# Optimization experiments

Measured on AMD Instinct MI355X. Metric: run time of the kernel, lower is better.

Reference implementation:

```python
import jax, jax.numpy as jnp
import numpy as np

B, N = 32, 4096
SA1 = (512, 0.2, 32)   # npoint, radius, nsample
SA2 = (128, 0.4, 64)
MLP1 = [3, 64, 64, 128]
MLP2 = [131, 128, 128, 256]   # 128 feats + 3 relative xyz
MLP3 = [259, 256, 512, 1024]  # 256 feats + 3 xyz (group_all)


def _mk_mlp(key, dims, prefix, d):
    for i in range(len(dims) - 1):
        key, k1 = jax.random.split(key)
        d[f"{prefix}_w{i}"] = jax.random.normal(k1, (dims[i], dims[i + 1]), jnp.float32) * (1.0 / np.sqrt(dims[i]))
        d[f"{prefix}_b{i}"] = jnp.zeros((dims[i + 1],), jnp.float32)
    return key


def setup_inputs() -> dict:
    key = jax.random.key(0)
    d = {}
    key, kx = jax.random.split(key)
    d["xyz"] = jax.random.uniform(kx, (B, N, 3), jnp.float32)  # normalized coords in [0,1)
    key = _mk_mlp(key, MLP1, "sa1", d)
    key = _mk_mlp(key, MLP2, "sa2", d)
    key = _mk_mlp(key, MLP3, "sa3", d)
    key, k1, k2 = jax.random.split(key, 3)
    d["cls_w"] = jax.random.normal(k1, (1024, 1), jnp.float32) * 0.03
    d["cls_b"] = jnp.zeros((1,), jnp.float32)
    d["reg_w"] = jax.random.normal(k2, (1024, 4), jnp.float32) * 0.03
    d["reg_b"] = jnp.zeros((4,), jnp.float32)
    return d


def fps(xyz, npoint):
    """Farthest point sampling. xyz: (B,N,3) -> idx (B,npoint) int32."""
    Bb, Nn, _ = xyz.shape

    def step(carry, _):
        dist, farthest = carry  # (B,N), (B,)
        centroid = jnp.take_along_axis(xyz, farthest[:, None, None], axis=1)  # (B,1,3)
        d = jnp.sum((xyz - centroid) ** 2, axis=-1)  # (B,N)
        dist = jnp.minimum(dist, d)
        nxt = jnp.argmax(dist, axis=-1).astype(jnp.int32)
        return (dist, nxt), farthest

    init = (jnp.full((Bb, Nn), 1e10, xyz.dtype), jnp.zeros((Bb,), jnp.int32))
    _, idx = jax.lax.scan(step, init, None, length=npoint)
    return idx.T  # (B,npoint)


def ball_query(radius, nsample, xyz, new_xyz):
    """xyz: (B,N,3), new_xyz: (B,S,3) -> idx (B,S,nsample) int32."""
    Bb, S, _ = new_xyz.shape
    Nn = xyz.shape[1]
    sqr = jnp.sum((new_xyz[:, :, None, :] - xyz[:, None, :, :]) ** 2, axis=-1)  # (B,S,N)
    idx = jnp.broadcast_to(jnp.arange(Nn, dtype=jnp.int32), (Bb, S, Nn))
    idx = jnp.where(sqr > radius * radius, Nn, idx)
    idx = jnp.sort(idx, axis=-1)[:, :, :nsample]
    first = idx[:, :, :1]
    return jnp.where(idx == Nn, first, idx)  # pad out-of-ball slots with first neighbor


def _sa(xyz, feats, npoint, radius, nsample, ws, bs):
    Bb = xyz.shape[0]
    cidx = fps(xyz, npoint)
    new_xyz = xyz[jnp.arange(Bb)[:, None], cidx]  # (B,S,3)
    gidx = ball_query(radius, nsample, xyz, new_xyz)  # (B,S,K)
    b3 = jnp.arange(Bb)[:, None, None]
    g = xyz[b3, gidx] - new_xyz[:, :, None, :]  # (B,S,K,3) relative coords
    if feats is not None:
        g = jnp.concatenate([g, feats[b3, gidx]], axis=-1)
    for w, b in zip(ws, bs):
        g = jax.nn.relu(g @ w + b)
    return new_xyz, jnp.max(g, axis=2)  # (B,S,C_out)


def _sa_all(xyz, feats, ws, bs):
    g = jnp.concatenate([xyz, feats], axis=-1)[:, None]  # (B,1,S,3+C)
    for w, b in zip(ws, bs):
        g = jax.nn.relu(g @ w + b)
    return jnp.max(g, axis=2)[:, 0]  # (B,C_out)


def reference(xyz, sa1_w0, sa1_b0, sa1_w1, sa1_b1, sa1_w2, sa1_b2,
              sa2_w0, sa2_b0, sa2_w1, sa2_b1, sa2_w2, sa2_b2,
              sa3_w0, sa3_b0, sa3_w1, sa3_b1, sa3_w2, sa3_b2,
              cls_w, cls_b, reg_w, reg_b):
    xyz1, f1 = _sa(xyz, None, SA1[0], SA1[1], SA1[2],
                   [sa1_w0, sa1_w1, sa1_w2], [sa1_b0, sa1_b1, sa1_b2])
    xyz2, f2 = _sa(xyz1, f1, SA2[0], SA2[1], SA2[2],
                   [sa2_w0, sa2_w1, sa2_w2], [sa2_b0, sa2_b1, sa2_b2])
    feat = _sa_all(xyz2, f2, [sa3_w0, sa3_w1, sa3_w2], [sa3_b0, sa3_b1, sa3_b2])  # (B,1024)
    return feat @ cls_w + cls_b, feat @ reg_w + reg_b
```

## Files before the change

kernel.cpp:

```cpp
#include <hip/hip_runtime.h>

#define DEVINL __device__ __forceinline__

typedef __attribute__((ext_vector_type(8))) short bf16x8;
typedef __attribute__((ext_vector_type(8))) unsigned short u16x8;
typedef __attribute__((ext_vector_type(4))) float f32x4;

DEVINL unsigned short f2bh(float f){
  unsigned u = __float_as_uint(f);
  return (unsigned short)((u + 0x7FFFu + ((u >> 16) & 1u)) >> 16);
}
DEVINL float bh2f(unsigned short h){ return __uint_as_float(((unsigned)h) << 16); }

DEVINL unsigned long long dpp_max_u64(unsigned long long k) {
#define DPP_STEP(ctrl)                                                        \
  {                                                                           \
    int hi = (int)(k >> 32), lo = (int)(unsigned)k;                           \
    int oh = __builtin_amdgcn_update_dpp(0, hi, ctrl, 0xF, 0xF, 1);           \
    int ol = __builtin_amdgcn_update_dpp(0, lo, ctrl, 0xF, 0xF, 1);           \
    unsigned long long ok =                                                   \
        ((unsigned long long)(unsigned)oh << 32) | (unsigned)ol;              \
    if (ok > k) k = ok;                                                       \
  }
  DPP_STEP(0x111)
  DPP_STEP(0x112)
  DPP_STEP(0x114)
  DPP_STEP(0x118)
  DPP_STEP(0x142)
  DPP_STEP(0x143)
#undef DPP_STEP
  return k;
}

template<int N, int NP, int NT>
DEVINL void fps_body(const float* __restrict__ xyz, float* __restrict__ nxyz,
                     int b, int t) {
  constexpr int PTS = N / NT;
  constexpr int NW = NT / 64;
  __shared__ float xs[N], ys[N], zs[N];
  __shared__ int farr[NP];
  __shared__ unsigned long long sk[2][(NW > 1 ? NW : 1)];
  float px[PTS], py[PTS], pz[PTS], dst[PTS];
  const float* base = xyz + (size_t)b * N * 3;
#pragma unroll
  for (int j = 0; j < PTS; ++j) {
    int i = t + j * NT;
    float x = base[i * 3 + 0], y = base[i * 3 + 1], z = base[i * 3 + 2];
    px[j] = x; py[j] = y; pz[j] = z;
    xs[i] = x; ys[i] = y; zs[i] = z;
    dst[j] = 1e10f;
  }
  if constexpr (NW > 1) __syncthreads();
  int far = 0;
  const int wv = t >> 6, ln = t & 63;
  for (int s = 0; s < NP; ++s) {
    float cx = xs[far], cy = ys[far], cz = zs[far];
    if (t == 0) farr[s] = far;
    float bv = -1.f; int bi = 0;
#pragma unroll
    for (int j = 0; j < PTS; ++j) {
      float dx = __fsub_rn(px[j], cx), dy = __fsub_rn(py[j], cy), dz = __fsub_rn(pz[j], cz);
      float d = __fadd_rn(__fadd_rn(__fmul_rn(dx, dx), __fmul_rn(dy, dy)), __fmul_rn(dz, dz));
      float nd = fminf(dst[j], d);
      dst[j] = nd;
      int i = t + j * NT;
      if (nd > bv) { bv = nd; bi = i; }
    }
    unsigned long long key =
        ((unsigned long long)__float_as_uint(bv) << 32) | (unsigned)(~bi);
    key = dpp_max_u64(key);
    if constexpr (NW == 1) {
      int rl = __builtin_amdgcn_readlane((int)(unsigned)key, 63);
      far = (int)(~(unsigned)rl);
    } else {
      const int p = s & 1;
      if (ln == 63) sk[p][wv] = key;
      __syncthreads();
      unsigned long long m = sk[p][0];
#pragma unroll
      for (int q = 1; q < NW; ++q) {
        unsigned long long qk = sk[p][q];
        if (qk > m) m = qk;
      }
      far = (int)(~(unsigned)m);
    }
  }
  if constexpr (NW > 1) __syncthreads();
  for (int s2 = t; s2 < NP; s2 += NT) {
    int fi = farr[s2];
    float* o = nxyz + ((size_t)b * NP + s2) * 3;
    o[0] = xs[fi]; o[1] = ys[fi]; o[2] = zs[fi];
  }
}

template<int N, int NS>
DEVINL void bq_body(const float* __restrict__ pts, const float* __restrict__ centers,
                    int* __restrict__ gidx, int Q, float r2, int blk, int t) {
  const int wv = t >> 6, ln = t & 63;
  const int g = blk * 4 + wv;
  const int b = g / Q, q = g % Q;
  const float* pb = pts + (size_t)b * N * 3;
  const float* c = centers + ((size_t)b * Q + q) * 3;
  const float cx = c[0], cy = c[1], cz = c[2];
  __shared__ int gbuf[4][NS];
  int taken = 0;
  for (int base = 0; base < N; base += 64) {
    if (taken >= NS) break;
    int i = base + ln;
    float dx = __fsub_rn(pb[i * 3 + 0], cx), dy = __fsub_rn(pb[i * 3 + 1], cy),
          dz = __fsub_rn(pb[i * 3 + 2], cz);
    float d = __fadd_rn(__fadd_rn(__fmul_rn(dx, dx), __fmul_rn(dy, dy)), __fmul_rn(dz, dz));
    bool in = (d <= r2);
    unsigned long long mk = __ballot(in);
    int rank = __popcll(mk & ((1ull << ln) - 1ull));
    int pos = taken + rank;
    if (in && pos < NS) gbuf[wv][pos] = i;
    taken += (int)__popcll(mk);
  }
  int total = taken < NS ? taken : NS;
  int first = gbuf[wv][0];
  int* out = gidx + ((size_t)b * Q + q) * NS;
  for (int j = ln; j < NS; j += 64) out[j] = (j < total) ? gbuf[wv][j] : first;
}

struct WPEnt { const float* W; unsigned short* hi; unsigned short* lo; int K, N, row0, beg, end; };
struct WPTab { WPEnt e[8]; };
DEVINL void wprep_body(const WPTab& tab, int idx) {
#pragma unroll
  for (int i = 0; i < 8; ++i) {
    const WPEnt& E = tab.e[i];
    if (idx >= E.beg && idx < E.end) {
      int local = idx - E.beg;
      int k = local / E.N, n = local - k * E.N;
      float v = E.W[(size_t)(E.row0 + k) * E.N + n];
      unsigned short h = f2bh(v);
      E.hi[(size_t)n * E.K + k] = h;
      E.lo[(size_t)n * E.K + k] = f2bh(v - bh2f(h));
    }
  }
}

__global__ __launch_bounds__(256) void fps1_wprep_kernel(const float* __restrict__ xyz,
                                                         float* __restrict__ nx1, WPTab tab) {
  if (blockIdx.x < 32) { fps_body<4096, 512, 256>(xyz, nx1, blockIdx.x, threadIdx.x); return; }
  wprep_body(tab, (blockIdx.x - 32) * 256 + threadIdx.x);
}

__global__ __launch_bounds__(256) void fps2_bq1_kernel(const float* __restrict__ xyz,
                                                       const float* __restrict__ nx1,
                                                       int* __restrict__ gidx1,
                                                       float* __restrict__ nx2, float r21) {
  if (blockIdx.x < 32) {
    if (threadIdx.x < 64) fps_body<512, 128, 64>(nx1, nx2, blockIdx.x, threadIdx.x);
    return;
  }
  bq_body<4096, 32>(xyz, nx1, gidx1, 512, r21, blockIdx.x - 32, threadIdx.x);
}

template<int K, int N, int AS, int WS, bool XYZC, int NTH>
DEVINL void do_layer(const unsigned short* __restrict__ Ghi, const unsigned short* __restrict__ Glo,
                     const float* __restrict__ Wxyz,
                     const float* __restrict__ A, unsigned short* __restrict__ Whi,
                     unsigned short* __restrict__ Wlo, const float* __restrict__ sxyz,
                     f32x4* acc, int t) {
  constexpr int KT = K / 32;
  constexpr int NCH = N / 64;
  constexpr int K8 = K / 8;
  constexpr int SI = (64 * K8) / NTH;
  const int l = t & 63, wv = t >> 6;

  u16x8 rh[SI], rl[SI];
#pragma unroll
  for (int s = 0; s < SI; ++s) {
    int u = t + s * NTH;
    int nn = u / K8, k8 = (u - nn * K8) * 8;
    rh[s] = *reinterpret_cast<const u16x8*>(Ghi + (size_t)nn * K + k8);
    rl[s] = *reinterpret_cast<const u16x8*>(Glo + (size_t)nn * K + k8);
  }

  bf16x8 ahi[KT], alo[KT];
  {
    const int row = wv * 16 + (l & 15);
    const float* ap = A + row * AS + (l >> 4) * 8;
#pragma unroll
    for (int kt = 0; kt < KT; ++kt) {
      float4 v0 = *reinterpret_cast<const float4*>(ap + kt * 32);
      float4 v1 = *reinterpret_cast<const float4*>(ap + kt * 32 + 4);
      float f[8] = {v0.x, v0.y, v0.z, v0.w, v1.x, v1.y, v1.z, v1.w};
      bf16x8 h, lo2;
#pragma unroll
      for (int j = 0; j < 8; ++j) {
        unsigned short hb = f2bh(f[j]);
        h[j] = (short)hb;
        lo2[j] = (short)f2bh(f[j] - bh2f(hb));
      }
      ahi[kt] = h; alo[kt] = lo2;
    }
  }
#pragma unroll
  for (int i = 0; i < N / 16; ++i) acc[i] = f32x4{0.f, 0.f, 0.f, 0.f};

#pragma unroll
  for (int c = 0; c < NCH; ++c) {
    __syncthreads();
#pragma unroll
    for (int s = 0; s < SI; ++s) {
      int u = t + s * NTH;
      int nn = u / K8, k8 = (u - nn * K8) * 8;
      *reinterpret_cast<u16x8*>(Whi + nn * WS + k8) = rh[s];
      *reinterpret_cast<u16x8*>(Wlo + nn * WS + k8) = rl[s];
    }
    if (c + 1 < NCH) {
#pragma unroll
      for (int s = 0; s < SI; ++s) {
        int u = t + s * NTH;
        int nn = u / K8, k8 = (u - nn * K8) * 8;
        rh[s] = *reinterpret_cast<const u16x8*>(Ghi + (size_t)((c + 1) * 64 + nn) * K + k8);
        rl[s] = *reinterpret_cast<const u16x8*>(Glo + (size_t)((c + 1) * 64 + nn) * K + k8);
      }
    }
    __syncthreads();
#pragma unroll
    for (int ct = 0; ct < 4; ++ct) {
      const unsigned short* wp = Whi + (ct * 16 + (l & 15)) * WS + (l >> 4) * 8;
      const unsigned short* wq = Wlo + (ct * 16 + (l & 15)) * WS + (l >> 4) * 8;
      f32x4 a = acc[c * 4 + ct];
#pragma unroll
      for (int kt = 0; kt < KT; ++kt) {
        bf16x8 wh = *reinterpret_cast<const bf16x8*>(wp + kt * 32);
        bf16x8 wl = *reinterpret_cast<const bf16x8*>(wq + kt * 32);
        a = __builtin_amdgcn_mfma_f32_16x16x32_bf16(ahi[kt], wh, a, 0, 0, 0);
        a = __builtin_amdgcn_mfma_f32_16x16x32_bf16(alo[kt], wh, a, 0, 0, 0);
        a = __builtin_amdgcn_mfma_f32_16x16x32_bf16(ahi[kt], wl, a, 0, 0, 0);
      }
      acc[c * 4 + ct] = a;
    }
  }
  if constexpr (XYZC) {
    float xr[4][3];
#pragma unroll
    for (int r = 0; r < 4; ++r) {
      int row = wv * 16 + (l >> 4) * 4 + r;
      xr[r][0] = sxyz[row * 4 + 0];
      xr[r][1] = sxyz[row * 4 + 1];
      xr[r][2] = sxyz[row * 4 + 2];
    }
#pragma unroll
    for (int gt = 0; gt < N / 16; ++gt) {
      int col = gt * 16 + (l & 15);
      float w0 = Wxyz[col], w1 = Wxyz[N + col], w2 = Wxyz[2 * N + col];
#pragma unroll
      for (int r = 0; r < 4; ++r)
        acc[gt][r] += xr[r][0] * w0 + xr[r][1] * w1 + xr[r][2] * w2;
    }
  }
}

template<int NPTS, int Q, int M, int GPB, int FD, int C1, int C2, int C3>
__global__ __launch_bounds__(512) void sa2_kernel(
    const float* __restrict__ pts, const float* __restrict__ centers,
    const int* __restrict__ gidx, const float* __restrict__ feats,
    const float* __restrict__ W0, const float* __restrict__ B0,
    const unsigned short* __restrict__ G0h, const unsigned short* __restrict__ G0l,
    const unsigned short* __restrict__ G1h, const unsigned short* __restrict__ G1l,
    const float* __restrict__ B1,
    const unsigned short* __restrict__ G2h, const unsigned short* __restrict__ G2l,
    const float* __restrict__ B2,
    float* __restrict__ fout) {
  constexpr int NTH = 512;
  constexpr int ROWS = M * GPB;
  constexpr int NWV = NTH / 64;
  static_assert(ROWS == 16 * NWV, "wave owns 16 rows");
  constexpr int MK1 = (FD > C1 ? FD : C1);
  constexpr int MAXK = (MK1 > C2 ? MK1 : C2);
  constexpr int AS = MAXK + 12;
  constexpr int WS = MAXK + 8;
  __shared__ __align__(16) float A[ROWS * AS];
  __shared__ __align__(16) unsigned short Whi[64 * WS];
  __shared__ __align__(16) unsigned short Wlo[64 * WS];
  __shared__ float sxyz[ROWS * 4];
  __shared__ int idxs[ROWS];
  __shared__ float ctr[GPB][4];
  __shared__ float red[NWV][C3];

  const int t = threadIdx.x;
  const int blk = blockIdx.x;
  const int b = blk / (Q / GPB);
  const int q0 = (blk % (Q / GPB)) * GPB;
  const int l = t & 63, wv = t >> 6;

  if (t < GPB * 3) {
    int g = t / 3, c2 = t % 3;
    ctr[g][c2] = centers[((size_t)b * Q + q0 + g) * 3 + c2];
  }
  for (int m = t; m < ROWS; m += NTH)
    idxs[m] = gidx[((size_t)b * Q + q0 + (m / M)) * M + (m % M)];
  __syncthreads();
  const float* pb = pts + (size_t)b * NPTS * 3;
  for (int m = t; m < ROWS; m += NTH) {
    int g = m / M, i = idxs[m];
    sxyz[m * 4 + 0] = pb[i * 3 + 0] - ctr[g][0];
    sxyz[m * 4 + 1] = pb[i * 3 + 1] - ctr[g][1];
    sxyz[m * 4 + 2] = pb[i * 3 + 2] - ctr[g][2];
  }
  {
    const int m = t >> 2, co = (t & 3) * (FD / 4);
    const float* src = feats + ((size_t)b * NPTS + idxs[m]) * FD + co;
    float* dst = A + m * AS + co;
#pragma unroll
    for (int j = 0; j < FD / 4; j += 4)
      *reinterpret_cast<float4*>(dst + j) = *reinterpret_cast<const float4*>(src + j);
  }
  __syncthreads();

  f32x4 acc[C3 / 16];

  do_layer<FD, C1, AS, WS, true, NTH>(G0h, G0l, W0, A, Whi, Wlo, sxyz, acc, t);
#pragma unroll
  for (int gt = 0; gt < C1 / 16; ++gt) {
    int col = gt * 16 + (l & 15);
    float bia = B0[col];
#pragma unroll
    for (int r = 0; r < 4; ++r)
      A[(wv * 16 + (l >> 4) * 4 + r) * AS + col] = fmaxf(acc[gt][r] + bia, 0.f);
  }

  do_layer<C1, C2, AS, WS, false, NTH>(G1h, G1l, nullptr, A, Whi, Wlo, sxyz, acc, t);
#pragma unroll
  for (int gt = 0; gt < C2 / 16; ++gt) {
    int col = gt * 16 + (l & 15);
    float bia = B1[col];
#pragma unroll
    for (int r = 0; r < 4; ++r)
      A[(wv * 16 + (l >> 4) * 4 + r) * AS + col] = fmaxf(acc[gt][r] + bia, 0.f);
  }

  do_layer<C2, C3, AS, WS, false, NTH>(G2h, G2l, nullptr, A, Whi, Wlo, sxyz, acc, t);
#pragma unroll
  for (int gt = 0; gt < C3 / 16; ++gt) {
    int col = gt * 16 + (l & 15);
    float v = fmaxf(fmaxf(acc[gt][0], acc[gt][1]), fmaxf(acc[gt][2], acc[gt][3]));
    v = fmaxf(v, __shfl_xor(v, 16, 64));
    v = fmaxf(v, __shfl_xor(v, 32, 64));
    if (l < 16) red[wv][col] = v + B2[col];
  }
  __syncthreads();
  constexpr int WPG = NWV / GPB;
  for (int u = t; u < GPB * C3; u += NTH) {
    int g = u / C3, c2 = u - g * C3;
    float v = red[g * WPG][c2];
#pragma unroll
    for (int w = 1; w < WPG; ++w) v = fmaxf(v, red[g * WPG + w][c2]);
    fout[((size_t)b * Q + q0 + g) * C3 + c2] = fmaxf(v, 0.f);
  }
}

template<int NPTS, int Q, int M, int GPB, int TPB>
DEVINL void sa1_body(const float* __restrict__ pts, const float* __restrict__ centers,
                     const int* __restrict__ gidx,
                     const float* __restrict__ W0, const float* __restrict__ B0,
                     const unsigned short* __restrict__ G1h, const unsigned short* __restrict__ G1l,
                     const float* __restrict__ B1,
                     const unsigned short* __restrict__ G2h, const unsigned short* __restrict__ G2l,
                     const float* __restrict__ B2,
                     float* __restrict__ fout, int sblk, int t) {
  static_assert(M * GPB == 64, "");
  constexpr int C1 = 64, C2 = 64, C3 = 128;
  constexpr int AS = 76;
  constexpr int WS = 72;
  constexpr int NC = C2 + C3;
  __shared__ __align__(16) float A[64 * AS];
  __shared__ __align__(16) unsigned short Wh[NC * WS];
  __shared__ __align__(16) unsigned short Wl[NC * WS];
  __shared__ float sxyz[64 * 4];
  __shared__ int idxs[64];
  __shared__ float ctr[GPB][4];
  __shared__ float red[4][C3];

  const int l = t & 63, wv = t >> 6;

  for (int u = t; u < NC * 8; u += 256) {
    int col = u >> 3, k8 = (u & 7) * 8;
    const unsigned short* sh = (col < C2) ? G1h + (size_t)col * 64 + k8
                                          : G2h + (size_t)(col - C2) * 64 + k8;
    const unsigned short* sl = (col < C2) ? G1l + (size_t)col * 64 + k8
                                          : G2l + (size_t)(col - C2) * 64 + k8;
    *reinterpret_cast<u16x8*>(Wh + col * WS + k8) = *reinterpret_cast<const u16x8*>(sh);
    *reinterpret_cast<u16x8*>(Wl + col * WS + k8) = *reinterpret_cast<const u16x8*>(sl);
  }

  for (int it = 0; it < TPB; ++it) {
    const int blk = sblk * TPB + it;
    const int b = blk / (Q / GPB);
    const int q0 = (blk % (Q / GPB)) * GPB;

    if (t < GPB * 3) {
      int g = t / 3, c2 = t % 3;
      ctr[g][c2] = centers[((size_t)b * Q + q0 + g) * 3 + c2];
    }
    for (int m = t; m < 64; m += 256)
      idxs[m] = gidx[((size_t)b * Q + q0 + (m / M)) * M + (m % M)];
    __syncthreads();
    const float* pb = pts + (size_t)b * NPTS * 3;
    for (int m = t; m < 64; m += 256) {
      int g = m / M, i = idxs[m];
      sxyz[m * 4 + 0] = pb[i * 3 + 0] - ctr[g][0];
      sxyz[m * 4 + 1] = pb[i * 3 + 1] - ctr[g][1];
      sxyz[m * 4 + 2] = pb[i * 3 + 2] - ctr[g][2];
    }
    __syncthreads();

    for (int u = t; u < 64 * C1; u += 256) {
      int m = u / C1, c2 = u - m * C1;
      float v = B0[c2] + sxyz[m * 4 + 0] * W0[0 * C1 + c2]
                       + sxyz[m * 4 + 1] * W0[1 * C1 + c2]
                       + sxyz[m * 4 + 2] * W0[2 * C1 + c2];
      A[m * AS + c2] = fmaxf(v, 0.f);
    }
    __syncthreads();

    f32x4 acc[8];
    {
      bf16x8 ah[2], al[2];
      const float* ap = A + (wv * 16 + (l & 15)) * AS + (l >> 4) * 8;
#pragma unroll
      for (int kt = 0; kt < 2; ++kt) {
        float4 v0 = *reinterpret_cast<const float4*>(ap + kt * 32);
        float4 v1 = *reinterpret_cast<const float4*>(ap + kt * 32 + 4);
        float f[8] = {v0.x, v0.y, v0.z, v0.w, v1.x, v1.y, v1.z, v1.w};
        bf16x8 h, lo2;
#pragma unroll
        for (int j = 0; j < 8; ++j) {
          unsigned short hb = f2bh(f[j]);
          h[j] = (short)hb;
          lo2[j] = (short)f2bh(f[j] - bh2f(hb));
        }
        ah[kt] = h; al[kt] = lo2;
      }
#pragma unroll
      for (int i = 0; i < 4; ++i) acc[i] = f32x4{0.f, 0.f, 0.f, 0.f};
#pragma unroll
      for (int ct = 0; ct < 4; ++ct) {
        const unsigned short* wp = Wh + (ct * 16 + (l & 15)) * WS + (l >> 4) * 8;
        const unsigned short* wq = Wl + (ct * 16 + (l & 15)) * WS + (l >> 4) * 8;
        f32x4 a = acc[ct];
#pragma unroll
        for (int kt = 0; kt < 2; ++kt) {
          bf16x8 wh = *reinterpret_cast<const bf16x8*>(wp + kt * 32);
          bf16x8 wl = *reinterpret_cast<const bf16x8*>(wq + kt * 32);
          a = __builtin_amdgcn_mfma_f32_16x16x32_bf16(ah[kt], wh, a, 0, 0, 0);
          a = __builtin_amdgcn_mfma_f32_16x16x32_bf16(al[kt], wh, a, 0, 0, 0);
          a = __builtin_amdgcn_mfma_f32_16x16x32_bf16(ah[kt], wl, a, 0, 0, 0);
        }
        acc[ct] = a;
      }
#pragma unroll
      for (int gt = 0; gt < 4; ++gt) {
        int col = gt * 16 + (l & 15);
        float bia = B1[col];
#pragma unroll
        for (int r = 0; r < 4; ++r)
          A[(wv * 16 + (l >> 4) * 4 + r) * AS + col] = fmaxf(acc[gt][r] + bia, 0.f);
      }
    }

    {
      bf16x8 ah[2], al[2];
      const float* ap = A + (wv * 16 + (l & 15)) * AS + (l >> 4) * 8;
#pragma unroll
      for (int kt = 0; kt < 2; ++kt) {
        float4 v0 = *reinterpret_cast<const float4*>(ap + kt * 32);
        float4 v1 = *reinterpret_cast<const float4*>(ap + kt * 32 + 4);
        float f[8] = {v0.x, v0.y, v0.z, v0.w, v1.x, v1.y, v1.z, v1.w};
        bf16x8 h, lo2;
#pragma unroll
        for (int j = 0; j < 8; ++j) {
          unsigned short hb = f2bh(f[j]);
          h[j] = (short)hb;
          lo2[j] = (short)f2bh(f[j] - bh2f(hb));
        }
        ah[kt] = h; al[kt] = lo2;
      }
#pragma unroll
      for (int i = 0; i < 8; ++i) acc[i] = f32x4{0.f, 0.f, 0.f, 0.f};
#pragma unroll
      for (int gt = 0; gt < 8; ++gt) {
        const unsigned short* wp = Wh + (C2 + gt * 16 + (l & 15)) * WS + (l >> 4) * 8;
        const unsigned short* wq = Wl + (C2 + gt * 16 + (l & 15)) * WS + (l >> 4) * 8;
        f32x4 a = acc[gt];
#pragma unroll
        for (int kt = 0; kt < 2; ++kt) {
          bf16x8 wh = *reinterpret_cast<const bf16x8*>(wp + kt * 32);
          bf16x8 wl = *reinterpret_cast<const bf16x8*>(wq + kt * 32);
          a = __builtin_amdgcn_mfma_f32_16x16x32_bf16(ah[kt], wh, a, 0, 0, 0);
          a = __builtin_amdgcn_mfma_f32_16x16x32_bf16(al[kt], wh, a, 0, 0, 0);
          a = __builtin_amdgcn_mfma_f32_16x16x32_bf16(ah[kt], wl, a, 0, 0, 0);
        }
        acc[gt] = a;
      }
#pragma unroll
      for (int gt = 0; gt < 8; ++gt) {
        int col = gt * 16 + (l & 15);
        float v = fmaxf(fmaxf(acc[gt][0], acc[gt][1]), fmaxf(acc[gt][2], acc[gt][3]));
        v = fmaxf(v, __shfl_xor(v, 16, 64));
        v = fmaxf(v, __shfl_xor(v, 32, 64));
        if (l < 16) red[wv][col] = v + B2[col];
      }
    }
    __syncthreads();
    constexpr int WPG = 4 / GPB;
    for (int u = t; u < GPB * C3; u += 256) {
      int g = u / C3, c2 = u - g * C3;
      float v = red[g * WPG][c2];
#pragma unroll
      for (int w = 1; w < WPG; ++w) v = fmaxf(v, red[g * WPG + w][c2]);
      fout[((size_t)b * Q + q0 + g) * C3 + c2] = fmaxf(v, 0.f);
    }
    __syncthreads();
  }
}

__global__ __launch_bounds__(256) void bq2_sa1_kernel(
    const float* __restrict__ xyz, const float* __restrict__ nx1,
    const float* __restrict__ nx2, int* __restrict__ gidx2, float r22,
    const int* __restrict__ gidx1,
    const float* __restrict__ s1w0, const float* __restrict__ s1b0,
    const unsigned short* __restrict__ g11h, const unsigned short* __restrict__ g11l,
    const float* __restrict__ s1b1,
    const unsigned short* __restrict__ g12h, const unsigned short* __restrict__ g12l,
    const float* __restrict__ s1b2, float* __restrict__ f1) {
  if (blockIdx.x < 1024) {
    bq_body<512, 64>(nx1, nx2, gidx2, 128, r22, blockIdx.x, threadIdx.x);
    return;
  }
  sa1_body<4096, 512, 32, 2, 4>(xyz, nx1, gidx1, s1w0, s1b0, g11h, g11l, s1b1,
                                g12h, g12l, s1b2, f1, blockIdx.x - 1024, threadIdx.x);
}

constexpr int AS3 = 532;
DEVINL void sa3_frags(const float* __restrict__ A, int l, int KT, bf16x8* ahi, bf16x8* alo) {
  const float* ap = A + (l & 15) * AS3 + (l >> 4) * 8;
  for (int kt = 0; kt < KT; ++kt) {
    float4 v0 = *reinterpret_cast<const float4*>(ap + kt * 32);
    float4 v1 = *reinterpret_cast<const float4*>(ap + kt * 32 + 4);
    float f[8] = {v0.x, v0.y, v0.z, v0.w, v1.x, v1.y, v1.z, v1.w};
    bf16x8 h, lo2;
#pragma unroll
    for (int j = 0; j < 8; ++j) {
      unsigned short hb = f2bh(f[j]);
      h[j] = (short)hb;
      lo2[j] = (short)f2bh(f[j] - bh2f(hb));
    }
    ahi[kt] = h; alo[kt] = lo2;
  }
}

template<int K>
DEVINL void sa3_mm64(const unsigned short* __restrict__ Gh, const unsigned short* __restrict__ Gl,
                     int ncol0, int l, const bf16x8* ahi, const bf16x8* alo, f32x4* acc4) {
  constexpr int KT = K / 32;
#pragma unroll
  for (int ct = 0; ct < 4; ++ct) {
    const unsigned short* hp = Gh + (size_t)(ncol0 + ct * 16 + (l & 15)) * K + (l >> 4) * 8;
    const unsigned short* lp = Gl + (size_t)(ncol0 + ct * 16 + (l & 15)) * K + (l >> 4) * 8;
    f32x4 a = acc4[ct];
#pragma unroll
    for (int kt = 0; kt < KT; ++kt) {
      bf16x8 wh = *reinterpret_cast<const bf16x8*>(hp + kt * 32);
      bf16x8 wl = *reinterpret_cast<const bf16x8*>(lp + kt * 32);
      a = __builtin_amdgcn_mfma_f32_16x16x32_bf16(ahi[kt], wh, a, 0, 0, 0);
      a = __builtin_amdgcn_mfma_f32_16x16x32_bf16(alo[kt], wh, a, 0, 0, 0);
      a = __builtin_amdgcn_mfma_f32_16x16x32_bf16(ahi[kt], wl, a, 0, 0, 0);
    }
    acc4[ct] = a;
  }
}

__global__ __launch_bounds__(256) void sa3f_kernel(
    const float* __restrict__ nx2, const float* __restrict__ f2,
    const float* __restrict__ W0full,
    const unsigned short* __restrict__ G0h, const unsigned short* __restrict__ G0l,
    const float* __restrict__ B0,
    const unsigned short* __restrict__ G1h, const unsigned short* __restrict__ G1l,
    const float* __restrict__ B1,
    const unsigned short* __restrict__ G2h, const unsigned short* __restrict__ G2l,
    const float* __restrict__ B2,
    float* __restrict__ partial) {
  __shared__ __align__(16) float A[16 * AS3];
  __shared__ float sxyz[16][4];
  const int t = threadIdx.x, l = t & 63, w = t >> 6;
  const int b = blockIdx.x >> 3, rb = blockIdx.x & 7;
  const int row0 = rb * 16;
  {
    int r = t >> 4, cc = (t & 15) * 16;
    const float* src = f2 + ((size_t)b * 128 + row0 + r) * 256 + cc;
    float* dstp = A + r * AS3 + cc;
#pragma unroll
    for (int j = 0; j < 16; j += 4)
      *reinterpret_cast<float4*>(dstp + j) = *reinterpret_cast<const float4*>(src + j);
    if (t < 16) {
      const float* s = nx2 + ((size_t)b * 128 + row0 + t) * 3;
      sxyz[t][0] = s[0]; sxyz[t][1] = s[1]; sxyz[t][2] = s[2];
    }
  }
  __syncthreads();

  {
    bf16x8 ah[8], al[8];
    sa3_frags(A, l, 8, ah, al);
    __syncthreads();
    f32x4 acc[4];
#pragma unroll
    for (int i = 0; i < 4; ++i) acc[i] = f32x4{0.f, 0.f, 0.f, 0.f};
    sa3_mm64<256>(G0h, G0l, w * 64, l, ah, al, acc);
    float xr[4][3];
#pragma unroll
    for (int r = 0; r < 4; ++r) {
      int row = (l >> 4) * 4 + r;
      xr[r][0] = sxyz[row][0]; xr[r][1] = sxyz[row][1]; xr[r][2] = sxyz[row][2];
    }
#pragma unroll
    for (int ct = 0; ct < 4; ++ct) {
      int col = w * 64 + ct * 16 + (l & 15);
      float w0 = W0full[col], w1 = W0full[256 + col], w2 = W0full[512 + col];
      float bia = B0[col];
#pragma unroll
      for (int r = 0; r < 4; ++r) {
        int row = (l >> 4) * 4 + r;
        float v = acc[ct][r] + xr[r][0] * w0 + xr[r][1] * w1 + xr[r][2] * w2 + bia;
        A[row * AS3 + col] = fmaxf(v, 0.f);
      }
    }
    __syncthreads();
  }

  {
    bf16x8 ah[8], al[8];
    sa3_frags(A, l, 8, ah, al);
    __syncthreads();
    f32x4 acc[8];
#pragma unroll
    for (int i = 0; i < 8; ++i) acc[i] = f32x4{0.f, 0.f, 0.f, 0.f};
    sa3_mm64<256>(G1h, G1l, w * 128, l, ah, al, acc);
    sa3_mm64<256>(G1h, G1l, w * 128 + 64, l, ah, al, acc + 4);
#pragma unroll
    for (int cc = 0; cc < 8; ++cc) {
      int col = w * 128 + cc * 16 + (l & 15);
      float bia = B1[col];
#pragma unroll
      for (int r = 0; r < 4; ++r) {
        int row = (l >> 4) * 4 + r;
        A[row * AS3 + col] = fmaxf(acc[cc][r] + bia, 0.f);
      }
    }
    __syncthreads();
  }

  {
    bf16x8 ah[16], al[16];
    sa3_frags(A, l, 16, ah, al);
    float* pout = partial + ((size_t)(b * 8 + rb)) * 1024;
#pragma unroll
    for (int sub = 0; sub < 4; ++sub) {
      f32x4 acc[4];
#pragma unroll
      for (int i = 0; i < 4; ++i) acc[i] = f32x4{0.f, 0.f, 0.f, 0.f};
      sa3_mm64<512>(G2h, G2l, w * 256 + sub * 64, l, ah, al, acc);
#pragma unroll
      for (int ct = 0; ct < 4; ++ct) {
        int col = w * 256 + sub * 64 + ct * 16 + (l & 15);
        float v = fmaxf(fmaxf(acc[ct][0], acc[ct][1]), fmaxf(acc[ct][2], acc[ct][3]));
        v = fmaxf(v, __shfl_xor(v, 16, 64));
        v = fmaxf(v, __shfl_xor(v, 32, 64));
        if (l < 16) pout[col] = v + B2[col];
      }
    }
  }
}

__global__ __launch_bounds__(256) void heads_kernel(const float* __restrict__ partial,
                                                    const float* __restrict__ cw,
                                                    const float* __restrict__ cb,
                                                    const float* __restrict__ rw,
                                                    const float* __restrict__ rb,
                                                    float* __restrict__ out) {
  const int b = blockIdx.x, t = threadIdx.x;
  const float* pb = partial + (size_t)b * 8 * 1024;
  float a0 = 0, a1 = 0, a2 = 0, a3 = 0, a4 = 0;
  for (int k = t; k < 1024; k += 256) {
    float m = pb[k];
#pragma unroll
    for (int p = 1; p < 8; ++p) m = fmaxf(m, pb[p * 1024 + k]);
    float f = fmaxf(m, 0.f);
    a0 += f * cw[k];
    const float* r = rw + (size_t)k * 4;
    a1 += f * r[0]; a2 += f * r[1]; a3 += f * r[2]; a4 += f * r[3];
  }
#pragma unroll
  for (int m = 32; m >= 1; m >>= 1) {
    a0 += __shfl_xor(a0, m, 64); a1 += __shfl_xor(a1, m, 64);
    a2 += __shfl_xor(a2, m, 64); a3 += __shfl_xor(a3, m, 64);
    a4 += __shfl_xor(a4, m, 64);
  }
  __shared__ float red[4][5];
  const int wv = t >> 6, ln = t & 63;
  if (ln == 0) { red[wv][0] = a0; red[wv][1] = a1; red[wv][2] = a2; red[wv][3] = a3; red[wv][4] = a4; }
  __syncthreads();
  if (t == 0) {
    float s0 = red[0][0] + red[1][0] + red[2][0] + red[3][0];
    float s1 = red[0][1] + red[1][1] + red[2][1] + red[3][1];
    float s2 = red[0][2] + red[1][2] + red[2][2] + red[3][2];
    float s3 = red[0][3] + red[1][3] + red[2][3] + red[3][3];
    float s4 = red[0][4] + red[1][4] + red[2][4] + red[3][4];
    out[b] = s0 + cb[0];
    out[32 + b * 4 + 0] = s1 + rb[0];
    out[32 + b * 4 + 1] = s2 + rb[1];
    out[32 + b * 4 + 2] = s3 + rb[2];
    out[32 + b * 4 + 3] = s4 + rb[3];
  }
}

extern "C" void kernel_launch(void* const* d_in, const int* in_sizes, int n_in,
                              void* d_out, int out_size, void* d_ws, size_t ws_size,
                              hipStream_t stream) {
  (void)in_sizes; (void)n_in; (void)out_size; (void)ws_size;
  const float* xyz  = (const float*)d_in[0];
  const float* s1w0 = (const float*)d_in[1];  const float* s1b0 = (const float*)d_in[2];
  const float* s1w1 = (const float*)d_in[3];  const float* s1b1 = (const float*)d_in[4];
  const float* s1w2 = (const float*)d_in[5];  const float* s1b2 = (const float*)d_in[6];
  const float* s2w0 = (const float*)d_in[7];  const float* s2b0 = (const float*)d_in[8];
  const float* s2w1 = (const float*)d_in[9];  const float* s2b1 = (const float*)d_in[10];
  const float* s2w2 = (const float*)d_in[11]; const float* s2b2 = (const float*)d_in[12];
  const float* s3w0 = (const float*)d_in[13]; const float* s3b0 = (const float*)d_in[14];
  const float* s3w1 = (const float*)d_in[15]; const float* s3b1 = (const float*)d_in[16];
  const float* s3w2 = (const float*)d_in[17]; const float* s3b2 = (const float*)d_in[18];
  const float* clsw = (const float*)d_in[19]; const float* clsb = (const float*)d_in[20];
  const float* regw = (const float*)d_in[21]; const float* regb = (const float*)d_in[22];

  char* ws = (char*)d_ws;
  float* nx1   = (float*)(ws + 0);
  int*   gidx1 = (int*)  (ws + 196608);
  float* f1    = (float*)(ws + 2293760);
  float* nx2   = (float*)(ws + 10682368);
  int*   gidx2 = (int*)  (ws + 10731520);
  float* f2    = (float*)(ws + 11780096);

  unsigned short* wt = (unsigned short*)(ws + 20168704);
  unsigned short* g11h = wt;
  unsigned short* g11l = wt + 4096;
  unsigned short* g12h = wt + 8192;
  unsigned short* g12l = wt + 16384;
  unsigned short* g20h = wt + 24576;
  unsigned short* g20l = wt + 40960;
  unsigned short* g21h = wt + 57344;
  unsigned short* g21l = wt + 73728;
  unsigned short* g22h = wt + 90112;
  unsigned short* g22l = wt + 122880;
  unsigned short* g30h = (unsigned short*)(ws + 20480000);
  unsigned short* g30l = (unsigned short*)(ws + 20611072);
  unsigned short* g31h = (unsigned short*)(ws + 20742144);
  unsigned short* g31l = (unsigned short*)(ws + 21004288);
  unsigned short* g32h = (unsigned short*)(ws + 21266432);
  unsigned short* g32l = (unsigned short*)(ws + 22315008);
  float* partial = (float*)(ws + 23363584);

  const float r21 = (float)(0.2 * 0.2);
  const float r22 = (float)(0.4 * 0.4);

  WPTab tab;
  int off = 0;
  auto set = [&](int i, const float* W, unsigned short* hi, unsigned short* lo,
                 int K, int N, int row0) {
    tab.e[i] = WPEnt{W, hi, lo, K, N, row0, off, off + K * N};
    off += K * N;
  };
  set(0, s1w1, g11h, g11l, 64, 64, 0);
  set(1, s1w2, g12h, g12l, 64, 128, 0);
  set(2, s2w0, g20h, g20l, 128, 128, 3);
  set(3, s2w1, g21h, g21l, 128, 128, 0);
  set(4, s2w2, g22h, g22l, 128, 256, 0);
  set(5, s3w0, g30h, g30l, 256, 256, 3);
  set(6, s3w1, g31h, g31l, 256, 512, 0);
  set(7, s3w2, g32h, g32l, 512, 1024, 0);
  const int wblocks = (off + 255) / 256;

  fps1_wprep_kernel<<<32 + wblocks, 256, 0, stream>>>(xyz, nx1, tab);
  fps2_bq1_kernel<<<32 + 4096, 256, 0, stream>>>(xyz, nx1, gidx1, nx2, r21);
  bq2_sa1_kernel<<<1024 + 2048, 256, 0, stream>>>(
      xyz, nx1, nx2, gidx2, r22, gidx1,
      s1w0, s1b0, g11h, g11l, s1b1, g12h, g12l, s1b2, f1);
  sa2_kernel<512, 128, 64, 2, 128, 128, 128, 256><<<2048, 512, 0, stream>>>(
      nx1, nx2, gidx2, f1, s2w0, s2b0,
      g20h, g20l, g21h, g21l, s2b1, g22h, g22l, s2b2, f2);
  sa3f_kernel<<<256, 256, 0, stream>>>(nx2, f2, s3w0, g30h, g30l, s3b0,
                                       g31h, g31l, s3b1, g32h, g32l, s3b2, partial);
  heads_kernel<<<32, 256, 0, stream>>>(partial, clsw, clsb, regw, regb, (float*)d_out);
}
```

Before: 712.4 us.

## Tree-reduce FPS argmax, pack points as float4, widen SA weight chunks

The FPS loop now stores points as packed float4 in shared memory, so the centroid is fetched with a single load instead of three. The per-thread argmax over points is now a pairwise tree reduction instead of a serial compare chain, which shortens the dependency chain. Separately, the SA2 MLP layer stages weights in 128-column chunks instead of 64, halving the number of barrier-separated chunk iterations but doubling the weight shared memory. The SA1 launch processes more groups per block with half as many blocks. This raises LDS use and register pressure and may reduce occupancy.

```diff
diff --git a/kernel.cpp b/kernel.cpp
--- a/kernel.cpp
+++ b/kernel.cpp
@@ -37,7 +37,7 @@
                      int b, int t) {
   constexpr int PTS = N / NT;
   constexpr int NW = NT / 64;
-  __shared__ float xs[N], ys[N], zs[N];
+  __shared__ __align__(16) float4 pts4[N];
   __shared__ int farr[NP];
   __shared__ unsigned long long sk[2][(NW > 1 ? NW : 1)];
   float px[PTS], py[PTS], pz[PTS], dst[PTS];
@@ -47,25 +47,32 @@
     int i = t + j * NT;
     float x = base[i * 3 + 0], y = base[i * 3 + 1], z = base[i * 3 + 2];
     px[j] = x; py[j] = y; pz[j] = z;
-    xs[i] = x; ys[i] = y; zs[i] = z;
+    pts4[i] = float4{x, y, z, 0.f};
     dst[j] = 1e10f;
   }
   if constexpr (NW > 1) __syncthreads();
   int far = 0;
   const int wv = t >> 6, ln = t & 63;
   for (int s = 0; s < NP; ++s) {
-    float cx = xs[far], cy = ys[far], cz = zs[far];
+    float4 c4 = pts4[far];
+    float cx = c4.x, cy = c4.y, cz = c4.z;
     if (t == 0) farr[s] = far;
-    float bv = -1.f; int bi = 0;
+    float v[PTS]; int ix[PTS];
 #pragma unroll
     for (int j = 0; j < PTS; ++j) {
       float dx = __fsub_rn(px[j], cx), dy = __fsub_rn(py[j], cy), dz = __fsub_rn(pz[j], cz);
       float d = __fadd_rn(__fadd_rn(__fmul_rn(dx, dx), __fmul_rn(dy, dy)), __fmul_rn(dz, dz));
       float nd = fminf(dst[j], d);
       dst[j] = nd;
-      int i = t + j * NT;
-      if (nd > bv) { bv = nd; bi = i; }
-    }
+      v[j] = nd; ix[j] = j;
+    }
+#pragma unroll
+    for (int off = 1; off < PTS; off <<= 1)
+#pragma unroll
+      for (int m = 0; m < PTS; m += 2 * off)
+        if (v[m + off] > v[m]) { v[m] = v[m + off]; ix[m] = ix[m + off]; }
+    float bv = v[0];
+    int bi = t + ix[0] * NT;
     unsigned long long key =
         ((unsigned long long)__float_as_uint(bv) << 32) | (unsigned)(~bi);
     key = dpp_max_u64(key);
@@ -87,9 +94,9 @@
   }
   if constexpr (NW > 1) __syncthreads();
   for (int s2 = t; s2 < NP; s2 += NT) {
-    int fi = farr[s2];
+    float4 p = pts4[farr[s2]];
     float* o = nxyz + ((size_t)b * NP + s2) * 3;
-    o[0] = xs[fi]; o[1] = ys[fi]; o[2] = zs[fi];
+    o[0] = p.x; o[1] = p.y; o[2] = p.z;
   }
 }
 
@@ -157,16 +164,17 @@
   bq_body<4096, 32>(xyz, nx1, gidx1, 512, r21, blockIdx.x - 32, threadIdx.x);
 }
 
-template<int K, int N, int AS, int WS, bool XYZC, int NTH>
+template<int K, int N, int CW, int AS, int WS, bool XYZC, int NTH>
 DEVINL void do_layer(const unsigned short* __restrict__ Ghi, const unsigned short* __restrict__ Glo,
                      const float* __restrict__ Wxyz,
                      const float* __restrict__ A, unsigned short* __restrict__ Whi,
                      unsigned short* __restrict__ Wlo, const float* __restrict__ sxyz,
                      f32x4* acc, int t) {
   constexpr int KT = K / 32;
-  constexpr int NCH = N / 64;
+  constexpr int NCH = N / CW;
   constexpr int K8 = K / 8;
-  constexpr int SI = (64 * K8) / NTH;
+  constexpr int SI = (CW * K8) / NTH;
+  constexpr int CT = CW / 16;
   const int l = t & 63, wv = t >> 6;
 
   u16x8 rh[SI], rl[SI];
@@ -215,16 +223,16 @@
       for (int s = 0; s < SI; ++s) {
         int u = t + s * NTH;
         int nn = u / K8, k8 = (u - nn * K8) * 8;
-        rh[s] = *reinterpret_cast<const u16x8*>(Ghi + (size_t)((c + 1) * 64 + nn) * K + k8);
-        rl[s] = *reinterpret_cast<const u16x8*>(Glo + (size_t)((c + 1) * 64 + nn) * K + k8);
-      }
-    }
-    __syncthreads();
-#pragma unroll
-    for (int ct = 0; ct < 4; ++ct) {
+        rh[s] = *reinterpret_cast<const u16x8*>(Ghi + (size_t)((c + 1) * CW + nn) * K + k8);
+        rl[s] = *reinterpret_cast<const u16x8*>(Glo + (size_t)((c + 1) * CW + nn) * K + k8);
+      }
+    }
+    __syncthreads();
+#pragma unroll
+    for (int ct = 0; ct < CT; ++ct) {
       const unsigned short* wp = Whi + (ct * 16 + (l & 15)) * WS + (l >> 4) * 8;
       const unsigned short* wq = Wlo + (ct * 16 + (l & 15)) * WS + (l >> 4) * 8;
-      f32x4 a = acc[c * 4 + ct];
+      f32x4 a = acc[c * CT + ct];
 #pragma unroll
       for (int kt = 0; kt < KT; ++kt) {
         bf16x8 wh = *reinterpret_cast<const bf16x8*>(wp + kt * 32);
@@ -233,7 +241,7 @@
         a = __builtin_amdgcn_mfma_f32_16x16x32_bf16(alo[kt], wh, a, 0, 0, 0);
         a = __builtin_amdgcn_mfma_f32_16x16x32_bf16(ahi[kt], wl, a, 0, 0, 0);
       }
-      acc[c * 4 + ct] = a;
+      acc[c * CT + ct] = a;
     }
   }
   if constexpr (XYZC) {
@@ -275,9 +283,10 @@
   constexpr int MAXK = (MK1 > C2 ? MK1 : C2);
   constexpr int AS = MAXK + 12;
   constexpr int WS = MAXK + 8;
+  constexpr int CW = 128;
   __shared__ __align__(16) float A[ROWS * AS];
-  __shared__ __align__(16) unsigned short Whi[64 * WS];
-  __shared__ __align__(16) unsigned short Wlo[64 * WS];
+  __shared__ __align__(16) unsigned short Whi[CW * WS];
+  __shared__ __align__(16) unsigned short Wlo[CW * WS];
   __shared__ float sxyz[ROWS * 4];
   __shared__ int idxs[ROWS];
   __shared__ float ctr[GPB][4];
@@ -315,7 +324,7 @@
 
   f32x4 acc[C3 / 16];
 
-  do_layer<FD, C1, AS, WS, true, NTH>(G0h, G0l, W0, A, Whi, Wlo, sxyz, acc, t);
+  do_layer<FD, C1, CW, AS, WS, true, NTH>(G0h, G0l, W0, A, Whi, Wlo, sxyz, acc, t);
 #pragma unroll
   for (int gt = 0; gt < C1 / 16; ++gt) {
     int col = gt * 16 + (l & 15);
@@ -325,7 +334,7 @@
       A[(wv * 16 + (l >> 4) * 4 + r) * AS + col] = fmaxf(acc[gt][r] + bia, 0.f);
   }
 
-  do_layer<C1, C2, AS, WS, false, NTH>(G1h, G1l, nullptr, A, Whi, Wlo, sxyz, acc, t);
+  do_layer<C1, C2, CW, AS, WS, false, NTH>(G1h, G1l, nullptr, A, Whi, Wlo, sxyz, acc, t);
 #pragma unroll
   for (int gt = 0; gt < C2 / 16; ++gt) {
     int col = gt * 16 + (l & 15);
@@ -335,7 +344,7 @@
       A[(wv * 16 + (l >> 4) * 4 + r) * AS + col] = fmaxf(acc[gt][r] + bia, 0.f);
   }
 
-  do_layer<C2, C3, AS, WS, false, NTH>(G2h, G2l, nullptr, A, Whi, Wlo, sxyz, acc, t);
+  do_layer<C2, C3, CW, AS, WS, false, NTH>(G2h, G2l, nullptr, A, Whi, Wlo, sxyz, acc, t);
 #pragma unroll
   for (int gt = 0; gt < C3 / 16; ++gt) {
     int col = gt * 16 + (l & 15);
@@ -533,7 +542,7 @@
     bq_body<512, 64>(nx1, nx2, gidx2, 128, r22, blockIdx.x, threadIdx.x);
     return;
   }
-  sa1_body<4096, 512, 32, 2, 4>(xyz, nx1, gidx1, s1w0, s1b0, g11h, g11l, s1b1,
+  sa1_body<4096, 512, 32, 2, 8>(xyz, nx1, gidx1, s1w0, s1b0, g11h, g11l, s1b1,
                                 g12h, g12l, s1b2, f1, blockIdx.x - 1024, threadIdx.x);
 }
 
@@ -786,7 +795,7 @@
 
   fps1_wprep_kernel<<<32 + wblocks, 256, 0, stream>>>(xyz, nx1, tab);
   fps2_bq1_kernel<<<32 + 4096, 256, 0, stream>>>(xyz, nx1, gidx1, nx2, r21);
-  bq2_sa1_kernel<<<1024 + 2048, 256, 0, stream>>>(
+  bq2_sa1_kernel<<<1024 + 1024, 256, 0, stream>>>(
       xyz, nx1, nx2, gidx2, r22, gidx1,
       s1w0, s1b0, g11h, g11l, s1b1, g12h, g12l, s1b2, f1);
   sa2_kernel<512, 128, 64, 2, 128, 128, 128, 256><<<2048, 512, 0, stream>>>(
```

New measurement: 731.5 us. +2.7%, slower.
